# Performance work log

Hardware: AMD Instinct MI355X
Metric: run time of the kernel (lower is better)

## Reference

```python
import jax, jax.numpy as jnp
import numpy as np

EMBED_DIM = 512  # channels C
B, H, W = 2, 64, 64


def _conv1x1(x, w, b):
    # x: [B, C, H, W]; w: [C_out, C_in]; b: [C_out]  (1x1 conv == per-pixel linear)
    return jnp.einsum('bchw,dc->bdhw', x, w) + b[None, :, None, None]


def setup_inputs() -> dict:
    key = jax.random.key(0)
    ks = jax.random.split(key, 9)
    C = EMBED_DIM
    s = 1.0 / np.sqrt(C)
    x = jax.random.normal(ks[0], (B, C, H, W), dtype=jnp.float32)
    wq = jax.random.normal(ks[1], (C, C), dtype=jnp.float32) * s
    bq = jax.random.normal(ks[2], (C,), dtype=jnp.float32) * 0.01
    wk = jax.random.normal(ks[3], (C, C), dtype=jnp.float32) * s
    bk = jax.random.normal(ks[4], (C,), dtype=jnp.float32) * 0.01
    wv = jax.random.normal(ks[5], (C, C), dtype=jnp.float32) * s
    bv = jax.random.normal(ks[6], (C,), dtype=jnp.float32) * 0.01
    wo = jax.random.normal(ks[7], (C, C), dtype=jnp.float32) * s
    bo = jax.random.normal(ks[8], (C,), dtype=jnp.float32) * 0.01
    return {"x": x, "wq": wq, "bq": bq, "wk": wk, "bk": bk,
            "wv": wv, "bv": bv, "wo": wo, "bo": bo}


def reference(x, wq, bq, wk, bk, wv, bv, wo, bo):
    b, c, h, w = x.shape
    n = h * w
    q = _conv1x1(x, wq, bq).reshape(b, c, n)
    k = _conv1x1(x, wk, bk).reshape(b, c, n)
    v = _conv1x1(x, wv, bv).reshape(b, c, n)
    # scores = q^T @ k over channel dim -> [b, n, n]; scale by sqrt(C) (scale=True)
    scores = jnp.einsum('bcn,bcm->bnm', q, k) / jnp.sqrt(jnp.asarray(c, x.dtype))
    attn = jax.nn.softmax(scores, axis=-1)
    # output = v @ attn^T -> [b, c, n]
    out = jnp.einsum('bcm,bnm->bcn', v, attn).reshape(b, c, h, w)
    return _conv1x1(out, wo, bo)
```

## Files before the change

### kernel.cpp

```cpp
#include <hip/hip_runtime.h>
#include <stdint.h>

typedef short s16x8 __attribute__((ext_vector_type(8)));
typedef unsigned short u16x8 __attribute__((ext_vector_type(8)));
typedef float f32x4 __attribute__((ext_vector_type(4)));

__device__ __forceinline__ float bf2f(unsigned short u) {
  union { unsigned u; float f; } c; c.u = ((unsigned)u) << 16; return c.f;
}
__device__ __forceinline__ unsigned short f2bf(float f) {
  union { float f; unsigned u; } c; c.f = f;
  unsigned u = c.u + 0x7fffu + ((c.u >> 16) & 1u);
  return (unsigned short)(u >> 16);
}

__device__ __forceinline__ void g2l16(const void* g, void* l) {
  __builtin_amdgcn_global_load_lds(
      (const __attribute__((address_space(1))) void*)(unsigned long long)g,
      (__attribute__((address_space(3))) void*)(unsigned)(unsigned long long)l,
      16, 0, 0);
}

template <int MODE>
__global__ __launch_bounds__(256) void gemm_abt(
    const unsigned short* __restrict__ A, int lda,
    const unsigned short* __restrict__ Bt, int ldb,
    unsigned short* __restrict__ C, int ldc,
    const float* __restrict__ bias,
    float* __restrict__ rowsum,
    int M, int N, int K, int nsplit,
    long long sA, long long sBt, long long sC, long long sSplit,
    float scale)
{
  __shared__ __align__(16) unsigned short smem[128 * 136];
  unsigned short* As = smem;
  unsigned short* Bs = smem + 128 * 64;

  const int ks = blockIdx.z % nsplit;
  const int bz = blockIdx.z / nsplit;
  A  += (long long)bz * sA;
  Bt += (long long)bz * sBt;
  C  += (long long)bz * sC + (long long)ks * sSplit;

  const int tile_m = blockIdx.y * 128;
  const int tile_n = blockIdx.x * 128;

  const int tid  = threadIdx.x;
  const int wid  = tid >> 6;
  const int lane = tid & 63;
  const int wm = (wid >> 1) * 64;
  const int wn = (wid & 1) * 64;
  const int lr = lane & 15;
  const int lq = lane >> 4;

  const int srow = lane >> 3;
  const int scol = ((lane & 7) ^ (srow & 7)) * 8;

  f32x4 acc[4][4];
  const f32x4 zero4 = {0.f, 0.f, 0.f, 0.f};
  #pragma unroll
  for (int i = 0; i < 4; ++i)
    #pragma unroll
    for (int j = 0; j < 4; ++j) acc[i][j] = zero4;

  const unsigned short* Arow = A  + (long long)tile_m * lda;
  const unsigned short* Brow = Bt + (long long)tile_n * ldb;

  const int kLen = K / nsplit;
  const int kBeg = ks * kLen;

  for (int k0 = kBeg; k0 < kBeg + kLen; k0 += 64) {
    #pragma unroll
    for (int c = 0; c < 4; ++c) {
      const int chunk = wid * 4 + c;
      const int row = chunk * 8 + srow;
      g2l16(Arow + (long long)row * lda + k0 + scol, As + chunk * 512);
      g2l16(Brow + (long long)row * ldb + k0 + scol, Bs + chunk * 512);
    }
    __syncthreads();
    #pragma unroll
    for (int kss = 0; kss < 2; ++kss) {
      const int cch = kss * 4 + lq;
      s16x8 af[4], bfr[4];
      #pragma unroll
      for (int i = 0; i < 4; ++i) {
        const int row = wm + i * 16 + lr;
        af[i] = *(const s16x8*)&As[row * 64 + ((cch ^ (row & 7)) * 8)];
      }
      #pragma unroll
      for (int j = 0; j < 4; ++j) {
        const int row = wn + j * 16 + lr;
        bfr[j] = *(const s16x8*)&Bs[row * 64 + ((cch ^ (row & 7)) * 8)];
      }
      #pragma unroll
      for (int i = 0; i < 4; ++i)
        #pragma unroll
        for (int j = 0; j < 4; ++j)
          acc[i][j] = __builtin_amdgcn_mfma_f32_16x16x32_bf16(af[i], bfr[j], acc[i][j], 0, 0, 0);
    }
    __syncthreads();
  }

  #pragma unroll
  for (int i = 0; i < 4; ++i) {
    const int lrow0 = wm + i * 16 + lq * 4;
    float rsum[4] = {0.f, 0.f, 0.f, 0.f};
    #pragma unroll
    for (int j = 0; j < 4; ++j) {
      const int lcol = wn + j * 16 + lr;
      float bcol = 0.f;
      if (MODE == 1 && bias) bcol = bias[tile_n + lcol];
      #pragma unroll
      for (int r = 0; r < 4; ++r) {
        float v = acc[i][j][r] * scale + bcol;
        if (MODE == 2) { v = __expf(v); rsum[r] += v; }
        smem[(lrow0 + r) * 136 + lcol] = f2bf(v);
      }
    }
    if (MODE == 2) {
      #pragma unroll
      for (int r = 0; r < 4; ++r) {
        float s = rsum[r];
        s += __shfl_xor(s, 1); s += __shfl_xor(s, 2);
        s += __shfl_xor(s, 4); s += __shfl_xor(s, 8);
        if (lr == 0)
          atomicAdd(&rowsum[(long long)bz * M + tile_m + lrow0 + r], s);
      }
    }
  }
  __syncthreads();
  const int row = tid >> 1;
  const int cb = (tid & 1) * 64;
  #pragma unroll
  for (int k = 0; k < 8; ++k) {
    u16x8 v = *(const u16x8*)&smem[row * 136 + cb + k * 8];
    *(u16x8*)&C[(long long)(tile_m + row) * ldc + tile_n + cb + k * 8] = v;
  }
}

__global__ __launch_bounds__(256) void cvt_weights(
    const float* __restrict__ wq, const float* __restrict__ wk,
    const float* __restrict__ wv, const float* __restrict__ wo,
    const float* __restrict__ bq, const float* __restrict__ bk,
    unsigned short* __restrict__ W3, unsigned short* __restrict__ wvT_b,
    unsigned short* __restrict__ wo_b, float* __restrict__ bqk3,
    float* __restrict__ rowsum, int n)
{
  const int i = blockIdx.x * 256 + threadIdx.x;
  if (i < n) {
    W3[i]      = f2bf(wq[i]);
    W3[n + i]  = f2bf(wk[i]);
    wvT_b[i]   = f2bf(wv[(i & 511) * 512 + (i >> 9)]);
    wo_b[i]    = f2bf(wo[i]);
  }
  if (i < 512) {
    bqk3[i]        = bq[i];
    bqk3[512 + i]  = bk[i];
    bqk3[1024 + i] = 0.f;
  }
  if (i < 8192) rowsum[i] = 0.f;
}

__global__ __launch_bounds__(256) void bias_pp(
    const float* __restrict__ wo, const float* __restrict__ bv,
    const float* __restrict__ bo, float* __restrict__ bpp)
{
  const int w = threadIdx.x >> 6, lane = threadIdx.x & 63;
  const int d = blockIdx.x * 4 + w;
  const float* row = wo + (long long)d * 512;
  float s = 0.f;
  #pragma unroll
  for (int c = 0; c < 512; c += 64) s += row[c + lane] * bv[c + lane];
  #pragma unroll
  for (int o = 32; o > 0; o >>= 1) s += __shfl_xor(s, o, 64);
  if (lane == 0) bpp[d] = s + bo[d];
}

__global__ __launch_bounds__(256) void transpose_cn(
    const float* __restrict__ x, unsigned short* __restrict__ xT,
    int C, int N)
{
  __shared__ float tile[32][33];
  const long long boff = (long long)blockIdx.z * C * N;
  const int n0 = blockIdx.x * 32;
  const int c0 = blockIdx.y * 32;
  const int tx = threadIdx.x;
  const int ty = threadIdx.y;
  #pragma unroll
  for (int k = 0; k < 32; k += 8)
    tile[ty + k][tx] = x[boff + (long long)(c0 + ty + k) * N + n0 + tx];
  __syncthreads();
  #pragma unroll
  for (int k = 0; k < 32; k += 8)
    xT[boff + (long long)(n0 + ty + k) * C + c0 + tx] = f2bf(tile[tx][ty + k]);
}

__global__ __launch_bounds__(256) void transpose_bf(
    const unsigned short* __restrict__ src, int srcLd, long long sSrc,
    unsigned short* __restrict__ dst, int dstLd, long long sDst,
    int R, int Cc)
{
  __shared__ unsigned short tile[32][33];
  const int r0 = blockIdx.x * 32;
  const int c0 = blockIdx.y * 32;
  const int tx = threadIdx.x;
  const int ty = threadIdx.y;
  const long long so = (long long)blockIdx.z * sSrc;
  const long long dofs = (long long)blockIdx.z * sDst;
  #pragma unroll
  for (int k = 0; k < 32; k += 8)
    tile[ty + k][tx] = src[so + (long long)(r0 + ty + k) * srcLd + c0 + tx];
  __syncthreads();
  #pragma unroll
  for (int k = 0; k < 32; k += 8)
    dst[dofs + (long long)(c0 + ty + k) * dstLd + r0 + tx] = tile[tx][ty + k];
}

__global__ __launch_bounds__(256) void reduce4_norm_out(
    const unsigned short* __restrict__ p, long long L,
    const float* __restrict__ rowsum, const float* __restrict__ bpp,
    float* __restrict__ o)
{
  const long long i = 8LL * (blockIdx.x * 256 + threadIdx.x);
  const int b = (int)(i >> 21);
  const int d = (int)((i >> 12) & 511);
  const int n = (int)(i & 4095);
  const float bb = bpp[d];
  const float* rs = &rowsum[b * 4096 + n];
  u16x8 a  = *(const u16x8*)&p[i];
  u16x8 b1 = *(const u16x8*)&p[L + i];
  u16x8 c  = *(const u16x8*)&p[2 * L + i];
  u16x8 d1 = *(const u16x8*)&p[3 * L + i];
  f32x4 o0, o1;
  #pragma unroll
  for (int j = 0; j < 4; ++j) {
    o0[j] = ((bf2f(a[j]) + bf2f(b1[j])) + (bf2f(c[j]) + bf2f(d1[j]))) / rs[j] + bb;
    o1[j] = ((bf2f(a[4 + j]) + bf2f(b1[4 + j])) + (bf2f(c[4 + j]) + bf2f(d1[4 + j]))) / rs[4 + j] + bb;
  }
  *(f32x4*)&o[i] = o0;
  *(f32x4*)&o[i + 4] = o1;
}

extern "C" void kernel_launch(void* const* d_in, const int* in_sizes, int n_in,
                              void* d_out, int out_size, void* d_ws, size_t ws_size,
                              hipStream_t stream) {
  (void)in_sizes; (void)n_in; (void)out_size; (void)ws_size;
  const float* x  = (const float*)d_in[0];
  const float* wq = (const float*)d_in[1];
  const float* bq = (const float*)d_in[2];
  const float* wk = (const float*)d_in[3];
  const float* bk = (const float*)d_in[4];
  const float* wv = (const float*)d_in[5];
  const float* bv = (const float*)d_in[6];
  const float* wo = (const float*)d_in[7];
  const float* bo = (const float*)d_in[8];
  float* out = (float*)d_out;

  const int Cc = 512, N = 4096, Bn = 2, C3 = 1536;
  const int CC = Cc * Cc;
  const long long NC  = (long long)N * Cc;
  const long long NC3 = (long long)N * C3;
  const long long NN  = (long long)N * N;

  char* wsb = (char*)d_ws;
  unsigned short* W3    = (unsigned short*)wsb;
  unsigned short* wvT_b = W3 + 3LL * CC;
  unsigned short* wo_b  = wvT_b + CC;
  float*          bqk3  = (float*)(wo_b + CC);
  float*          bpp   = bqk3 + 1536;
  float*          rsum  = bpp + 512;
  unsigned short* xT    = (unsigned short*)(rsum + 8192);
  unsigned short* qkvoT = xT + Bn * NC;
  unsigned short* vo    = qkvoT + Bn * NC3;
  unsigned short* S     = vo + Bn * NC;
  unsigned short* part  = S + Bn * NN;

  const float inv_sqrt_c = 0.044194173824159216f;

  cvt_weights<<<dim3((CC + 255) / 256), 256, 0, stream>>>(
      wq, wk, wv, wo, bq, bk, W3, wvT_b, wo_b, bqk3, rsum, CC);
  bias_pp<<<dim3(128), 256, 0, stream>>>(wo, bv, bo, bpp);
  gemm_abt<1><<<dim3(4, 4, 1), 256, 0, stream>>>(
      wo_b, 512, wvT_b, 512, W3 + 2LL * CC, 512, nullptr, nullptr,
      512, 512, 512, 1, 0, 0, 0, 0, 1.0f);
  transpose_cn<<<dim3(N / 32, Cc / 32, Bn), dim3(32, 8), 0, stream>>>(x, xT, Cc, N);

  gemm_abt<1><<<dim3(C3 / 128, N / 128, Bn), 256, 0, stream>>>(
      xT, Cc, W3, Cc, qkvoT, C3, bqk3, nullptr, N, C3, Cc, 1,
      NC, 0, NC3, 0, 1.0f);
  transpose_bf<<<dim3(N / 32, Cc / 32, Bn), dim3(32, 8), 0, stream>>>(
      qkvoT + 1024, C3, NC3, vo, N, NC, N, Cc);
  gemm_abt<2><<<dim3(N / 128, N / 128, Bn), 256, 0, stream>>>(
      qkvoT, C3, qkvoT + 512, C3, S, N, nullptr, rsum, N, N, Cc, 1,
      NC3, NC3, NN, 0, inv_sqrt_c);
  gemm_abt<1><<<dim3(N / 128, 4, Bn * 4), 256, 0, stream>>>(
      vo, N, S, N, part, N, nullptr, nullptr, 512, N, N, 4,
      NC, NN, NC, (long long)Bn * NC, 1.0f);
  reduce4_norm_out<<<dim3((int)((Bn * NC) / 2048)), 256, 0, stream>>>(
      part, (long long)Bn * NC, rsum, bpp, out);
}
```

Measured before the change: 264.1 us.

## Template GEMM on M tile height and use 256x128 tiles with 512 threads

Adds an M-tile template parameter to the bf16 MFMA GEMM, so the three large GEMMs use 256x128 output tiles computed by 8 waves instead of 128x128 by 4 waves. Each B tile staged in LDS is now shared across twice as many rows, which cuts redundant global and LDS traffic per output. The epilogue writes the taller tile back through LDS in two halves. The cost is a halved grid, with fewer blocks to spread across CUs, and larger LDS use per block.

```diff
diff --git a/kernel.cpp b/kernel.cpp
--- a/kernel.cpp
+++ b/kernel.cpp
@@ -21,8 +21,8 @@
       16, 0, 0);
 }
 
-template <int MODE>
-__global__ __launch_bounds__(256) void gemm_abt(
+template <int MODE, int MT>
+__global__ __launch_bounds__(2 * MT) void gemm_abt(
     const unsigned short* __restrict__ A, int lda,
     const unsigned short* __restrict__ Bt, int ldb,
     unsigned short* __restrict__ C, int ldc,
@@ -32,9 +32,12 @@
     long long sA, long long sBt, long long sC, long long sSplit,
     float scale)
 {
-  __shared__ __align__(16) unsigned short smem[128 * 136];
+  constexpr int STAGE_ELEMS  = (MT + 128) * 64;
+  constexpr int BOUNCE_ELEMS = 128 * 136;
+  constexpr int SMEM_ELEMS = STAGE_ELEMS > BOUNCE_ELEMS ? STAGE_ELEMS : BOUNCE_ELEMS;
+  __shared__ __align__(16) unsigned short smem[SMEM_ELEMS];
   unsigned short* As = smem;
-  unsigned short* Bs = smem + 128 * 64;
+  unsigned short* Bs = smem + MT * 64;
 
   const int ks = blockIdx.z % nsplit;
   const int bz = blockIdx.z / nsplit;
@@ -42,7 +45,7 @@
   Bt += (long long)bz * sBt;
   C  += (long long)bz * sC + (long long)ks * sSplit;
 
-  const int tile_m = blockIdx.y * 128;
+  const int tile_m = blockIdx.y * MT;
   const int tile_n = blockIdx.x * 128;
 
   const int tid  = threadIdx.x;
@@ -69,13 +72,22 @@
   const int kLen = K / nsplit;
   const int kBeg = ks * kLen;
 
+  constexpr int ACH   = MT / 8;
+  constexpr int NCH   = ACH + 16;
+  constexpr int NW    = MT / 32;
+  constexpr int PERW  = NCH / NW;
+
   for (int k0 = kBeg; k0 < kBeg + kLen; k0 += 64) {
     #pragma unroll
-    for (int c = 0; c < 4; ++c) {
-      const int chunk = wid * 4 + c;
-      const int row = chunk * 8 + srow;
-      g2l16(Arow + (long long)row * lda + k0 + scol, As + chunk * 512);
-      g2l16(Brow + (long long)row * ldb + k0 + scol, Bs + chunk * 512);
+    for (int c = 0; c < PERW; ++c) {
+      const int chunk = wid * PERW + c;
+      if (chunk < ACH) {
+        const int row = chunk * 8 + srow;
+        g2l16(Arow + (long long)row * lda + k0 + scol, smem + chunk * 512);
+      } else {
+        const int row = (chunk - ACH) * 8 + srow;
+        g2l16(Brow + (long long)row * ldb + k0 + scol, smem + chunk * 512);
+      }
     }
     __syncthreads();
     #pragma unroll
@@ -101,40 +113,84 @@
     __syncthreads();
   }
 
-  #pragma unroll
-  for (int i = 0; i < 4; ++i) {
-    const int lrow0 = wm + i * 16 + lq * 4;
-    float rsum[4] = {0.f, 0.f, 0.f, 0.f};
-    #pragma unroll
-    for (int j = 0; j < 4; ++j) {
-      const int lcol = wn + j * 16 + lr;
-      float bcol = 0.f;
-      if (MODE == 1 && bias) bcol = bias[tile_n + lcol];
+  if (MODE == 2) {
+    #pragma unroll
+    for (int i = 0; i < 4; ++i) {
+      float rs[4] = {0.f, 0.f, 0.f, 0.f};
+      #pragma unroll
+      for (int j = 0; j < 4; ++j)
+        #pragma unroll
+        for (int r = 0; r < 4; ++r) {
+          acc[i][j][r] = __expf(acc[i][j][r] * scale);
+          rs[r] += acc[i][j][r];
+        }
       #pragma unroll
       for (int r = 0; r < 4; ++r) {
-        float v = acc[i][j][r] * scale + bcol;
-        if (MODE == 2) { v = __expf(v); rsum[r] += v; }
-        smem[(lrow0 + r) * 136 + lcol] = f2bf(v);
-      }
-    }
-    if (MODE == 2) {
-      #pragma unroll
-      for (int r = 0; r < 4; ++r) {
-        float s = rsum[r];
+        float s = rs[r];
         s += __shfl_xor(s, 1); s += __shfl_xor(s, 2);
         s += __shfl_xor(s, 4); s += __shfl_xor(s, 8);
         if (lr == 0)
-          atomicAdd(&rowsum[(long long)bz * M + tile_m + lrow0 + r], s);
-      }
-    }
-  }
-  __syncthreads();
-  const int row = tid >> 1;
-  const int cb = (tid & 1) * 64;
-  #pragma unroll
-  for (int k = 0; k < 8; ++k) {
-    u16x8 v = *(const u16x8*)&smem[row * 136 + cb + k * 8];
-    *(u16x8*)&C[(long long)(tile_m + row) * ldc + tile_n + cb + k * 8] = v;
+          atomicAdd(&rowsum[(long long)bz * M + tile_m + wm + i * 16 + lq * 4 + r], s);
+      }
+    }
+  }
+
+  if (MT == 128) {
+    #pragma unroll
+    for (int i = 0; i < 4; ++i) {
+      const int lrow0 = wm + i * 16 + lq * 4;
+      #pragma unroll
+      for (int j = 0; j < 4; ++j) {
+        const int lcol = wn + j * 16 + lr;
+        const float bcol = (MODE == 1 && bias) ? bias[tile_n + lcol] : 0.f;
+        #pragma unroll
+        for (int r = 0; r < 4; ++r) {
+          const float v = (MODE == 2) ? acc[i][j][r] : acc[i][j][r] * scale + bcol;
+          smem[(lrow0 + r) * 136 + lcol] = f2bf(v);
+        }
+      }
+    }
+    __syncthreads();
+    const int row = tid >> 1;
+    const int cb = (tid & 1) * 64;
+    #pragma unroll
+    for (int k = 0; k < 8; ++k) {
+      u16x8 v = *(const u16x8*)&smem[row * 136 + cb + k * 8];
+      *(u16x8*)&C[(long long)(tile_m + row) * ldc + tile_n + cb + k * 8] = v;
+    }
+  } else {
+    #pragma unroll
+    for (int p = 0; p < 2; ++p) {
+      if ((wm >> 7) == p) {
+        const int lwm = wm & 127;
+        #pragma unroll
+        for (int i = 0; i < 4; ++i) {
+          const int lrow0 = lwm + i * 16 + lq * 4;
+          #pragma unroll
+          for (int j = 0; j < 4; ++j) {
+            const int lcol = wn + j * 16 + lr;
+            const float bcol = (MODE == 1 && bias) ? bias[tile_n + lcol] : 0.f;
+            #pragma unroll
+            for (int r = 0; r < 4; ++r) {
+              const float v = (MODE == 2) ? acc[i][j][r] : acc[i][j][r] * scale + bcol;
+              smem[(lrow0 + r) * 136 + lcol] = f2bf(v);
+            }
+          }
+        }
+      }
+      __syncthreads();
+      if ((tid >> 8) == p) {
+        const int t2 = tid & 255;
+        const int row = t2 >> 1;
+        const int cb = (t2 & 1) * 64;
+        #pragma unroll
+        for (int k = 0; k < 8; ++k) {
+          u16x8 v = *(const u16x8*)&smem[row * 136 + cb + k * 8];
+          *(u16x8*)&C[(long long)(tile_m + p * 128 + row) * ldc + tile_n + cb + k * 8] = v;
+        }
+      }
+      if (p == 0) __syncthreads();
+    }
   }
 }
 
@@ -280,20 +336,20 @@
   cvt_weights<<<dim3((CC + 255) / 256), 256, 0, stream>>>(
       wq, wk, wv, wo, bq, bk, W3, wvT_b, wo_b, bqk3, rsum, CC);
   bias_pp<<<dim3(128), 256, 0, stream>>>(wo, bv, bo, bpp);
-  gemm_abt<1><<<dim3(4, 4, 1), 256, 0, stream>>>(
+  gemm_abt<1, 128><<<dim3(4, 4, 1), 256, 0, stream>>>(
       wo_b, 512, wvT_b, 512, W3 + 2LL * CC, 512, nullptr, nullptr,
       512, 512, 512, 1, 0, 0, 0, 0, 1.0f);
   transpose_cn<<<dim3(N / 32, Cc / 32, Bn), dim3(32, 8), 0, stream>>>(x, xT, Cc, N);
 
-  gemm_abt<1><<<dim3(C3 / 128, N / 128, Bn), 256, 0, stream>>>(
+  gemm_abt<1, 256><<<dim3(C3 / 128, N / 256, Bn), 512, 0, stream>>>(
       xT, Cc, W3, Cc, qkvoT, C3, bqk3, nullptr, N, C3, Cc, 1,
       NC, 0, NC3, 0, 1.0f);
   transpose_bf<<<dim3(N / 32, Cc / 32, Bn), dim3(32, 8), 0, stream>>>(
       qkvoT + 1024, C3, NC3, vo, N, NC, N, Cc);
-  gemm_abt<2><<<dim3(N / 128, N / 128, Bn), 256, 0, stream>>>(
+  gemm_abt<2, 256><<<dim3(N / 128, N / 256, Bn), 512, 0, stream>>>(
       qkvoT, C3, qkvoT + 512, C3, S, N, nullptr, rsum, N, N, Cc, 1,
       NC3, NC3, NN, 0, inv_sqrt_c);
-  gemm_abt<1><<<dim3(N / 128, 4, Bn * 4), 256, 0, stream>>>(
+  gemm_abt<1, 256><<<dim3(N / 128, 512 / 256, Bn * 4), 512, 0, stream>>>(
       vo, N, S, N, part, N, nullptr, nullptr, 512, N, N, 4,
       NC, NN, NC, (long long)Bn * NC, 1.0f);
   reduce4_norm_out<<<dim3((int)((Bn * NC) / 2048)), 256, 0, stream>>>(
```

After: 253.4 us. 1.04x faster.
